# Performance work log

Hardware: AMD Instinct MI355X
Metric: run time of the kernel (lower is better)

## Reference

```python
import jax, jax.numpy as jnp
import numpy as np

N = 20000            # nodes
E = 320000           # edges (before self loops)
NUM_PLAYERS = 5000
FEAT = 64            # feature_dim
H = 128              # hidden_dim
OUT = 10             # out_features
NEG_SLOPE = 0.2


def _p(key, shape, fan_in):
    return jax.random.normal(key, shape, dtype=jnp.float32) / np.sqrt(fan_in)


def setup_inputs() -> dict:
    key = jax.random.key(0)
    ks = jax.random.split(key, 20)
    # x_player: col 0 = player id (stored as float), cols 1: = features
    ids = jax.random.randint(ks[0], (N, 1), 0, NUM_PLAYERS + 1).astype(jnp.float32)
    feats = jax.random.normal(ks[1], (N, FEAT), dtype=jnp.float32)
    x_player = jnp.concatenate([ids, feats], axis=1)
    edge_index = jax.random.randint(ks[2], (2, E), 0, N, dtype=jnp.int32)
    return {
        "x_player": x_player,
        "edge_index": edge_index,
        "emb": jax.random.normal(ks[3], (NUM_PLAYERS + 1, H), dtype=jnp.float32),
        "proj_W": _p(ks[4], (H + FEAT, H), H + FEAT),
        "proj_b": jnp.zeros((H,), jnp.float32),
        "W1l": _p(ks[5], (H, 4 * H), H),
        "W1r": _p(ks[6], (H, 4 * H), H),
        "att1": _p(ks[7], (4, H), H),
        "b1": jnp.zeros((4 * H,), jnp.float32),
        "W2l": _p(ks[8], (4 * H, H), 4 * H),
        "W2r": _p(ks[9], (4 * H, H), 4 * H),
        "att2": _p(ks[10], (1, H), H),
        "b2": jnp.zeros((H,), jnp.float32),
        "out_W": _p(ks[11], (H, OUT), H),
        "out_b": jnp.zeros((OUT,), jnp.float32),
    }


def gatv2(x, src, dst, Wl, Wr, att, bias, heads, ch, concat):
    # GATv2Conv (PyG defaults: share_weights=False, negative_slope=0.2,
    # add_self_loops handled by caller, dropout off at eval)
    xl = (x @ Wl).reshape(N, heads, ch)   # source transform (x_j)
    xr = (x @ Wr).reshape(N, heads, ch)   # target transform (x_i)
    h = xl[src] + xr[dst]                                      # [E,H,C]
    e = jnp.sum(jax.nn.leaky_relu(h, NEG_SLOPE) * att, -1)     # [E,H]
    # segment softmax over incoming edges of each dst node
    m = jax.ops.segment_max(e, dst, num_segments=N)            # [N,H]
    ex = jnp.exp(e - m[dst])
    s = jax.ops.segment_sum(ex, dst, num_segments=N)
    alpha = ex / (s[dst] + 1e-16)                              # [E,H]
    out = jax.ops.segment_sum(alpha[..., None] * xl[src], dst, num_segments=N)
    out = out.reshape(N, heads * ch) if concat else out.mean(axis=1)
    return out + bias


def reference(x_player, edge_index, emb, proj_W, proj_b,
              W1l, W1r, att1, b1, W2l, W2r, att2, b2, out_W, out_b):
    ids = x_player[:, 0].astype(jnp.int32)
    combined = jnp.concatenate([emb[ids], x_player[:, 1:]], axis=1)
    x = jax.nn.relu(combined @ proj_W + proj_b)                # [N,H]
    # add self loops (GATv2Conv default)
    loop = jnp.arange(N, dtype=edge_index.dtype)
    src = jnp.concatenate([edge_index[0], loop])
    dst = jnp.concatenate([edge_index[1], loop])
    x = jax.nn.relu(gatv2(x, src, dst, W1l, W1r, att1, b1, 4, H, True))
    x = gatv2(x, src, dst, W2l, W2r, att2, b2, 1, H, True)
    return x @ out_W + out_b                                   # [N,OUT]
```

## Files before the change

kernel.cpp:

```cpp
#include <hip/hip_runtime.h>
#include <math.h>

#define NNODES 20000
#define XP_COLS 65

typedef unsigned int uint32;
typedef __attribute__((ext_vector_type(8))) short short8;
typedef __attribute__((ext_vector_type(4))) float float4v;

__device__ __forceinline__ float bflo(uint32 u){ return __uint_as_float(u << 16); }
__device__ __forceinline__ float bfhi(uint32 u){ return __uint_as_float(u & 0xffff0000u); }
__device__ __forceinline__ unsigned short f2bf(float f){
  uint32 u = __float_as_uint(f);
  uint32 r = (u + 0x7fffu + ((u >> 16) & 1u)) >> 16;
  return (unsigned short)r;
}
__device__ __forceinline__ void unpack8(uint4 u, float* x){
  x[0]=bflo(u.x); x[1]=bfhi(u.x); x[2]=bflo(u.y); x[3]=bfhi(u.y);
  x[4]=bflo(u.z); x[5]=bfhi(u.z); x[6]=bflo(u.w); x[7]=bfhi(u.w);
}

__global__ void k_count(const int* __restrict__ dst, int E, int* __restrict__ deg){
  int e = blockIdx.x * 256 + threadIdx.x;
  if (e < E) atomicAdd(&deg[dst[e]], 1);
}

__global__ __launch_bounds__(256) void k_scan(const int* __restrict__ deg,
                                              int* __restrict__ off,
                                              int* __restrict__ cursor){
  const int CH = 80;
  int tid = threadIdx.x;
  int lane = tid & 63, w = tid >> 6;
  int beg = tid * CH;
  bool act = beg < NNODES;
  int sum = 0;
  if (act){
    const int4* p = (const int4*)(deg + beg);
    #pragma unroll
    for (int i = 0; i < 20; i++){
      int4 v = p[i];
      sum += v.x + v.y + v.z + v.w + 4;
    }
  }
  int inc = sum;
  #pragma unroll
  for (int d = 1; d < 64; d <<= 1){
    int t = __shfl_up(inc, d, 64);
    if (lane >= d) inc += t;
  }
  __shared__ int wtot[4];
  if (lane == 63) wtot[w] = inc;
  __syncthreads();
  int wbase = 0;
  for (int i = 0; i < w; i++) wbase += wtot[i];
  int run = wbase + inc - sum;
  if (act){
    const int4* p = (const int4*)(deg + beg);
    int4* po = (int4*)(off + beg);
    int4* pc = (int4*)(cursor + beg);
    #pragma unroll
    for (int i = 0; i < 20; i++){
      int4 v = p[i];
      int4 o;
      o.x = run; run += v.x + 1;
      o.y = run; run += v.y + 1;
      o.z = run; run += v.z + 1;
      o.w = run; run += v.w + 1;
      po[i] = o; pc[i] = o;
    }
  }
  if (tid == 249) off[NNODES] = run;
}

__global__ void k_fill(const int* __restrict__ src, const int* __restrict__ dst, int E,
                       int* __restrict__ cursor, int* __restrict__ csr){
  int t = blockIdx.x * 256 + threadIdx.x;
  if (t < NNODES){
    int p = atomicAdd(&cursor[t], 1);
    csr[p] = t;
  } else if (t < NNODES + E){
    int e = t - NNODES;
    int p = atomicAdd(&cursor[dst[e]], 1);
    csr[p] = src[e];
  }
}

__global__ void k_cvt(const float* __restrict__ W1l, const float* __restrict__ W1r,
                      const float* __restrict__ W2l, const float* __restrict__ W2r,
                      const float* __restrict__ projW,
                      unsigned short* __restrict__ T1l, unsigned short* __restrict__ T1r,
                      unsigned short* __restrict__ T2l, unsigned short* __restrict__ T2r,
                      unsigned short* __restrict__ Tp){
  int idx = blockIdx.x * 256 + threadIdx.x;
  if (idx < 65536){
    int o = idx;
    int n = o >> 7, k = o & 127;
    T1l[o] = f2bf(W1l[k * 512 + n]);
  } else if (idx < 131072){
    int o = idx - 65536;
    int n = o >> 7, k = o & 127;
    T1r[o] = f2bf(W1r[k * 512 + n]);
  } else if (idx < 196608){
    int o = idx - 131072;
    int n = o >> 9, k = o & 511;
    T2l[o] = f2bf(W2l[k * 128 + n]);
  } else if (idx < 262144){
    int o = idx - 196608;
    int n = o >> 9, k = o & 511;
    T2r[o] = f2bf(W2r[k * 128 + n]);
  } else if (idx < 286720){
    int o = idx - 262144;
    int n = o / 192, k = o - n * 192;
    Tp[o] = f2bf(projW[k * 128 + n]);
  }
}

__global__ __launch_bounds__(256) void k_proj_mfma(const float* __restrict__ xp,
                                                   const float* __restrict__ emb,
                                                   const unsigned short* __restrict__ Bt,
                                                   const float* __restrict__ bias,
                                                   unsigned short* __restrict__ Xb){
  __shared__ unsigned short As[64][40];
  __shared__ unsigned short Bs[128][40];
  __shared__ int ids[64];
  int tid = threadIdx.x;
  int bm = blockIdx.x * 64;
  int w = tid >> 6, lane = tid & 63;
  int wm = (w >> 1) * 32, wn = (w & 1) * 64;
  int quad = lane >> 4, l16 = lane & 15;
  if (tid < 64){
    int g = bm + tid;
    ids[tid] = (g < NNODES) ? (int)xp[(size_t)g * XP_COLS] : 0;
  }
  float4v acc[2][4];
  #pragma unroll
  for (int i = 0; i < 2; i++)
    #pragma unroll
    for (int j = 0; j < 4; j++) acc[i][j] = (float4v){0.f,0.f,0.f,0.f};
  int am = tid >> 2, ak = (tid & 3) * 8;
  int gm = bm + am;
  bool mv = gm < NNODES;
  int brow = tid >> 1, bk = (tid & 1) * 16;
  __syncthreads();

  for (int k0 = 0; k0 < 192; k0 += 32){
    float v[8];
    if (k0 < 128){
      const float* ep = emb + (size_t)ids[am] * 128 + k0 + ak;
      float4 e0 = *(const float4*)ep;
      float4 e1 = *(const float4*)(ep + 4);
      v[0]=e0.x; v[1]=e0.y; v[2]=e0.z; v[3]=e0.w;
      v[4]=e1.x; v[5]=e1.y; v[6]=e1.z; v[7]=e1.w;
    } else {
      const float* fp = xp + (size_t)gm * XP_COLS + 1 + (k0 - 128) + ak;
      #pragma unroll
      for (int i = 0; i < 8; i++) v[i] = mv ? fp[i] : 0.f;
    }
    ushort4 o0, o1;
    o0.x=f2bf(v[0]); o0.y=f2bf(v[1]); o0.z=f2bf(v[2]); o0.w=f2bf(v[3]);
    o1.x=f2bf(v[4]); o1.y=f2bf(v[5]); o1.z=f2bf(v[6]); o1.w=f2bf(v[7]);
    *(ushort4*)&As[am][ak]     = o0;
    *(ushort4*)&As[am][ak + 4] = o1;
    const unsigned short* bp = Bt + (size_t)brow * 192 + k0 + bk;
    *(uint4*)&Bs[brow][bk]     = *(const uint4*)bp;
    *(uint4*)&Bs[brow][bk + 8] = *(const uint4*)(bp + 8);
    __syncthreads();
    short8 af[2], bf[4];
    #pragma unroll
    for (int t = 0; t < 2; t++) af[t] = *(const short8*)&As[wm + t * 16 + l16][quad * 8];
    #pragma unroll
    for (int t = 0; t < 4; t++) bf[t] = *(const short8*)&Bs[wn + t * 16 + l16][quad * 8];
    #pragma unroll
    for (int tm = 0; tm < 2; tm++)
      #pragma unroll
      for (int tn = 0; tn < 4; tn++)
        acc[tm][tn] = __builtin_amdgcn_mfma_f32_16x16x32_bf16(af[tm], bf[tn], acc[tm][tn], 0, 0, 0);
    __syncthreads();
  }
  #pragma unroll
  for (int tm = 0; tm < 2; tm++){
    #pragma unroll
    for (int r = 0; r < 4; r++){
      int row = bm + wm + tm * 16 + quad * 4 + r;
      if (row >= NNODES) continue;
      #pragma unroll
      for (int tn = 0; tn < 4; tn++){
        int col = wn + tn * 16 + l16;
        float val = fmaxf(acc[tm][tn][r] + bias[col], 0.f);
        Xb[(size_t)row * 128 + col] = f2bf(val);
      }
    }
  }
}

template<int K, int N, int MODE, int NH>
__global__ __launch_bounds__(256) void k_mfma(const unsigned short* __restrict__ A,
                                              const unsigned short* __restrict__ B0t,
                                              const unsigned short* __restrict__ B1t,
                                              void* __restrict__ C0, void* __restrict__ C1,
                                              const float* __restrict__ att,
                                              float* __restrict__ dl, float* __restrict__ dr){
  const unsigned short* Bt = blockIdx.z ? B1t : B0t;
  __shared__ unsigned short As[64][40];
  __shared__ unsigned short Bs[128][40];
  __shared__ float red[4][32];
  int tid = threadIdx.x;
  int bm = blockIdx.y * 64;
  int bn = blockIdx.x * 128;
  int head = (NH == 1) ? 0 : blockIdx.x;
  int w = tid >> 6, lane = tid & 63;
  int wm = (w >> 1) * 32, wn = (w & 1) * 64;
  int quad = lane >> 4, l16 = lane & 15;
  float av[4];
  #pragma unroll
  for (int tn = 0; tn < 4; tn++) av[tn] = att[head * 128 + wn + tn * 16 + l16];
  float4v acc[2][4];
  #pragma unroll
  for (int i = 0; i < 2; i++)
    #pragma unroll
    for (int j = 0; j < 4; j++) acc[i][j] = (float4v){0.f,0.f,0.f,0.f};
  int am = tid >> 2, ak = (tid & 3) * 8;
  int gm = bm + am;
  bool mv = gm < NNODES;
  int brow = tid >> 1, bk = (tid & 1) * 16;

  for (int k0 = 0; k0 < K; k0 += 32){
    uint4 va = {0u,0u,0u,0u};
    if (mv) va = *(const uint4*)(A + (size_t)gm * K + k0 + ak);
    *(uint4*)&As[am][ak] = va;
    const unsigned short* bp = Bt + (size_t)(bn + brow) * K + k0 + bk;
    *(uint4*)&Bs[brow][bk]     = *(const uint4*)bp;
    *(uint4*)&Bs[brow][bk + 8] = *(const uint4*)(bp + 8);
    __syncthreads();
    short8 af[2], bf[4];
    #pragma unroll
    for (int t = 0; t < 2; t++) af[t] = *(const short8*)&As[wm + t * 16 + l16][quad * 8];
    #pragma unroll
    for (int t = 0; t < 4; t++) bf[t] = *(const short8*)&Bs[wn + t * 16 + l16][quad * 8];
    #pragma unroll
    for (int tm = 0; tm < 2; tm++)
      #pragma unroll
      for (int tn = 0; tn < 4; tn++)
        acc[tm][tn] = __builtin_amdgcn_mfma_f32_16x16x32_bf16(af[tm], bf[tn], acc[tm][tn], 0, 0, 0);
    __syncthreads();
  }
  #pragma unroll
  for (int tm = 0; tm < 2; tm++){
    #pragma unroll
    for (int r = 0; r < 4; r++){
      int row = bm + wm + tm * 16 + quad * 4 + r;
      if (row < NNODES){
        #pragma unroll
        for (int tn = 0; tn < 4; tn++){
          int col = bn + wn + tn * 16 + l16;
          float val = acc[tm][tn][r];
          if (MODE == 0 || blockIdx.z == 0){
            unsigned short* C = (unsigned short*)(blockIdx.z ? C1 : C0);
            C[(size_t)row * N + col] = f2bf(val);
          } else {
            ((float*)C1)[(size_t)row * N + col] = val;
          }
        }
      }
      float pd = acc[tm][0][r] * av[0];
      pd = fmaf(acc[tm][1][r], av[1], pd);
      pd = fmaf(acc[tm][2][r], av[2], pd);
      pd = fmaf(acc[tm][3][r], av[3], pd);
      pd += __shfl_xor(pd, 1);
      pd += __shfl_xor(pd, 2);
      pd += __shfl_xor(pd, 4);
      pd += __shfl_xor(pd, 8);
      if (l16 == 0) red[w][tm * 16 + quad * 4 + r] = pd;
    }
  }
  __syncthreads();
  if (tid < 64){
    float v = (tid < 32) ? red[0][tid] + red[1][tid] : red[2][tid & 31] + red[3][tid & 31];
    int row = bm + tid;
    if (row < NNODES){
      float* D = blockIdx.z ? dr : dl;
      D[row * NH + head] = v;
    }
  }
}

__global__ __launch_bounds__(256) void k_attn1(const unsigned short* __restrict__ xl,
                                               const unsigned short* __restrict__ xr,
                                               const float* __restrict__ dl, const float* __restrict__ dr,
                                               const float* __restrict__ att, const float* __restrict__ bias,
                                               const int* __restrict__ off, const int* __restrict__ csr,
                                               unsigned short* __restrict__ out){
  int lane = threadIdx.x & 63;
  int n = blockIdx.x * 4 + (threadIdx.x >> 6);
  int h = lane >> 4;
  uint4 ur = *(const uint4*)(xr + (size_t)n * 512 + lane * 8);
  float r[8]; unpack8(ur, r);
  const float* ap = att + lane * 8;
  float4 A0 = *(const float4*)ap, A1 = *(const float4*)(ap + 4);
  float a[8] = {A0.x,A0.y,A0.z,A0.w,A1.x,A1.y,A1.z,A1.w};
  float c0 = 0.6f * dr[n * 4 + h];
  int beg = off[n], end = off[n + 1];

  float m = -INFINITY, s = 0.f;
  float acc[8] = {0,0,0,0,0,0,0,0};
  int j = beg;
  for (; j + 3 < end; j += 4){
    int sn0 = csr[j], sn1 = csr[j + 1], sn2 = csr[j + 2], sn3 = csr[j + 3];
    uint4 u0 = *(const uint4*)(xl + (size_t)sn0 * 512 + lane * 8);
    uint4 u1 = *(const uint4*)(xl + (size_t)sn1 * 512 + lane * 8);
    uint4 u2 = *(const uint4*)(xl + (size_t)sn2 * 512 + lane * 8);
    uint4 u3 = *(const uint4*)(xl + (size_t)sn3 * 512 + lane * 8);
    float d0 = dl[sn0 * 4 + h], d1 = dl[sn1 * 4 + h];
    float d2 = dl[sn2 * 4 + h], d3 = dl[sn3 * 4 + h];
    float x0[8], x1[8], x2[8], x3[8];
    unpack8(u0, x0); unpack8(u1, x1); unpack8(u2, x2); unpack8(u3, x3);
    float p0 = 0.f, p1 = 0.f, p2 = 0.f, p3 = 0.f;
    #pragma unroll
    for (int i = 0; i < 8; i++){
      p0 = fmaf(a[i], fabsf(x0[i] + r[i]), p0);
      p1 = fmaf(a[i], fabsf(x1[i] + r[i]), p1);
      p2 = fmaf(a[i], fabsf(x2[i] + r[i]), p2);
      p3 = fmaf(a[i], fabsf(x3[i] + r[i]), p3);
    }
    p0 += __shfl_xor(p0, 1); p1 += __shfl_xor(p1, 1); p2 += __shfl_xor(p2, 1); p3 += __shfl_xor(p3, 1);
    p0 += __shfl_xor(p0, 2); p1 += __shfl_xor(p1, 2); p2 += __shfl_xor(p2, 2); p3 += __shfl_xor(p3, 2);
    p0 += __shfl_xor(p0, 4); p1 += __shfl_xor(p1, 4); p2 += __shfl_xor(p2, 4); p3 += __shfl_xor(p3, 4);
    p0 += __shfl_xor(p0, 8); p1 += __shfl_xor(p1, 8); p2 += __shfl_xor(p2, 8); p3 += __shfl_xor(p3, 8);
    float e0 = fmaf(0.6f, d0, fmaf(0.4f, p0, c0));
    float e1 = fmaf(0.6f, d1, fmaf(0.4f, p1, c0));
    float e2 = fmaf(0.6f, d2, fmaf(0.4f, p2, c0));
    float e3 = fmaf(0.6f, d3, fmaf(0.4f, p3, c0));
    float emax = fmaxf(fmaxf(e0, e1), fmaxf(e2, e3));
    if (__any(emax > m)){
      float nm = fmaxf(m, emax);
      float al  = __expf(m - nm);
      float ex0 = __expf(e0 - nm), ex1 = __expf(e1 - nm);
      float ex2 = __expf(e2 - nm), ex3 = __expf(e3 - nm);
      m = nm;
      s = fmaf(s, al, (ex0 + ex1) + (ex2 + ex3));
      #pragma unroll
      for (int i = 0; i < 8; i++){
        float t = fmaf(ex0, x0[i], ex1 * x1[i]);
        t = fmaf(ex2, x2[i], t);
        t = fmaf(ex3, x3[i], t);
        acc[i] = fmaf(acc[i], al, t);
      }
    } else {
      float ex0 = __expf(e0 - m), ex1 = __expf(e1 - m);
      float ex2 = __expf(e2 - m), ex3 = __expf(e3 - m);
      s += (ex0 + ex1) + (ex2 + ex3);
      #pragma unroll
      for (int i = 0; i < 8; i++){
        float t = fmaf(ex0, x0[i], ex1 * x1[i]);
        t = fmaf(ex2, x2[i], t);
        acc[i] = fmaf(ex3, x3[i], acc[i] + t);
      }
    }
  }
  for (; j < end; j++){
    int sn = csr[j];
    float dls = dl[sn * 4 + h];
    uint4 ux = *(const uint4*)(xl + (size_t)sn * 512 + lane * 8);
    float x[8]; unpack8(ux, x);
    float p = 0.f;
    #pragma unroll
    for (int i = 0; i < 8; i++) p = fmaf(a[i], fabsf(x[i] + r[i]), p);
    p += __shfl_xor(p, 1);
    p += __shfl_xor(p, 2);
    p += __shfl_xor(p, 4);
    p += __shfl_xor(p, 8);
    float e = fmaf(0.6f, dls, fmaf(0.4f, p, c0));
    if (__any(e > m)){
      float nm = fmaxf(m, e);
      float al = __expf(m - nm);
      float ex = __expf(e - nm);
      m = nm;
      s = fmaf(s, al, ex);
      #pragma unroll
      for (int i = 0; i < 8; i++) acc[i] = fmaf(acc[i], al, ex * x[i]);
    } else {
      float ex = __expf(e - m);
      s += ex;
      #pragma unroll
      for (int i = 0; i < 8; i++) acc[i] = fmaf(ex, x[i], acc[i]);
    }
  }
  float inv = 1.f / (s + 1e-16f);
  const float* bp = bias + lane * 8;
  float4 B0 = *(const float4*)bp, B1 = *(const float4*)(bp + 4);
  float bb[8] = {B0.x,B0.y,B0.z,B0.w,B1.x,B1.y,B1.z,B1.w};
  unsigned short o[8];
  #pragma unroll
  for (int i = 0; i < 8; i++)
    o[i] = f2bf(fmaxf(fmaf(acc[i], inv, bb[i]), 0.f));
  uint4 ov;
  ov.x = (uint32)o[0] | ((uint32)o[1] << 16);
  ov.y = (uint32)o[2] | ((uint32)o[3] << 16);
  ov.z = (uint32)o[4] | ((uint32)o[5] << 16);
  ov.w = (uint32)o[6] | ((uint32)o[7] << 16);
  *(uint4*)(out + (size_t)n * 512 + lane * 8) = ov;
}

__global__ __launch_bounds__(256) void k_attn2(const unsigned short* __restrict__ xl,
                                               const float* __restrict__ xr,
                                               const float* __restrict__ dl, const float* __restrict__ dr,
                                               const float* __restrict__ att, const float* __restrict__ bias,
                                               const float* __restrict__ outW, const float* __restrict__ outb,
                                               const int* __restrict__ off, const int* __restrict__ csr,
                                               float* __restrict__ out){
  __shared__ float Wsh[1280];
  int tid = threadIdx.x;
  for (int i = tid; i < 1280; i += 256) Wsh[i] = outW[i];
  __syncthreads();
  int lane = tid & 63;
  int n = blockIdx.x * 4 + (tid >> 6);
  float2 rv = *(const float2*)(xr + (size_t)n * 128 + lane * 2);
  float2 av = *(const float2*)(att + lane * 2);
  float c0 = 0.6f * dr[n];
  int beg = off[n], end = off[n + 1];
  float m = -INFINITY, s = 0.f;
  float a0 = 0.f, a1 = 0.f;
  int j = beg;
  for (; j + 3 < end; j += 4){
    int sn0 = csr[j], sn1 = csr[j + 1], sn2 = csr[j + 2], sn3 = csr[j + 3];
    uint32 u0 = *(const uint32*)(xl + (size_t)sn0 * 128 + lane * 2);
    uint32 u1 = *(const uint32*)(xl + (size_t)sn1 * 128 + lane * 2);
    uint32 u2 = *(const uint32*)(xl + (size_t)sn2 * 128 + lane * 2);
    uint32 u3 = *(const uint32*)(xl + (size_t)sn3 * 128 + lane * 2);
    float d0 = dl[sn0], d1 = dl[sn1], d2 = dl[sn2], d3 = dl[sn3];
    float x00 = bflo(u0), x01 = bfhi(u0);
    float x10 = bflo(u1), x11 = bfhi(u1);
    float x20 = bflo(u2), x21 = bfhi(u2);
    float x30 = bflo(u3), x31 = bfhi(u3);
    float p0 = fmaf(av.x, fabsf(x00 + rv.x), av.y * fabsf(x01 + rv.y));
    float p1 = fmaf(av.x, fabsf(x10 + rv.x), av.y * fabsf(x11 + rv.y));
    float p2 = fmaf(av.x, fabsf(x20 + rv.x), av.y * fabsf(x21 + rv.y));
    float p3 = fmaf(av.x, fabsf(x30 + rv.x), av.y * fabsf(x31 + rv.y));
    p0 += __shfl_xor(p0, 1);  p1 += __shfl_xor(p1, 1);  p2 += __shfl_xor(p2, 1);  p3 += __shfl_xor(p3, 1);
    p0 += __shfl_xor(p0, 2);  p1 += __shfl_xor(p1, 2);  p2 += __shfl_xor(p2, 2);  p3 += __shfl_xor(p3, 2);
    p0 += __shfl_xor(p0, 4);  p1 += __shfl_xor(p1, 4);  p2 += __shfl_xor(p2, 4);  p3 += __shfl_xor(p3, 4);
    p0 += __shfl_xor(p0, 8);  p1 += __shfl_xor(p1, 8);  p2 += __shfl_xor(p2, 8);  p3 += __shfl_xor(p3, 8);
    p0 += __shfl_xor(p0, 16); p1 += __shfl_xor(p1, 16); p2 += __shfl_xor(p2, 16); p3 += __shfl_xor(p3, 16);
    p0 += __shfl_xor(p0, 32); p1 += __shfl_xor(p1, 32); p2 += __shfl_xor(p2, 32); p3 += __shfl_xor(p3, 32);
    float e0 = fmaf(0.6f, d0, fmaf(0.4f, p0, c0));
    float e1 = fmaf(0.6f, d1, fmaf(0.4f, p1, c0));
    float e2 = fmaf(0.6f, d2, fmaf(0.4f, p2, c0));
    float e3 = fmaf(0.6f, d3, fmaf(0.4f, p3, c0));
    float emax = fmaxf(fmaxf(e0, e1), fmaxf(e2, e3));
    if (emax > m){
      float al  = __expf(m - emax);
      float ex0 = __expf(e0 - emax), ex1 = __expf(e1 - emax);
      float ex2 = __expf(e2 - emax), ex3 = __expf(e3 - emax);
      m = emax;
      s  = fmaf(s,  al, (ex0 + ex1) + (ex2 + ex3));
      float t0 = fmaf(ex0, x00, ex1 * x10); t0 = fmaf(ex2, x20, t0); t0 = fmaf(ex3, x30, t0);
      float t1 = fmaf(ex0, x01, ex1 * x11); t1 = fmaf(ex2, x21, t1); t1 = fmaf(ex3, x31, t1);
      a0 = fmaf(a0, al, t0);
      a1 = fmaf(a1, al, t1);
    } else {
      float ex0 = __expf(e0 - m), ex1 = __expf(e1 - m);
      float ex2 = __expf(e2 - m), ex3 = __expf(e3 - m);
      s += (ex0 + ex1) + (ex2 + ex3);
      float t0 = fmaf(ex0, x00, ex1 * x10); t0 = fmaf(ex2, x20, t0);
      float t1 = fmaf(ex0, x01, ex1 * x11); t1 = fmaf(ex2, x21, t1);
      a0 = fmaf(ex3, x30, a0 + t0);
      a1 = fmaf(ex3, x31, a1 + t1);
    }
  }
  for (; j < end; j++){
    int sn = csr[j];
    float dls = dl[sn];
    uint32 u = *(const uint32*)(xl + (size_t)sn * 128 + lane * 2);
    float x0 = bflo(u), x1 = bfhi(u);
    float p = fmaf(av.x, fabsf(x0 + rv.x), av.y * fabsf(x1 + rv.y));
    p += __shfl_xor(p, 1);
    p += __shfl_xor(p, 2);
    p += __shfl_xor(p, 4);
    p += __shfl_xor(p, 8);
    p += __shfl_xor(p, 16);
    p += __shfl_xor(p, 32);
    float e = fmaf(0.6f, dls, fmaf(0.4f, p, c0));
    if (e > m){
      float al = __expf(m - e);
      m = e;
      s  = fmaf(s,  al, 1.f);
      a0 = fmaf(a0, al, x0);
      a1 = fmaf(a1, al, x1);
    } else {
      float ex = __expf(e - m);
      s += ex;
      a0 = fmaf(ex, x0, a0);
      a1 = fmaf(ex, x1, a1);
    }
  }
  float inv = 1.f / (s + 1e-16f);
  int c = lane * 2;
  float x2_0 = fmaf(a0, inv, bias[c]);
  float x2_1 = fmaf(a1, inv, bias[c + 1]);
  #pragma unroll
  for (int o = 0; o < 10; o++){
    float p = fmaf(x2_0, Wsh[c * 10 + o], x2_1 * Wsh[(c + 1) * 10 + o]);
    p += __shfl_xor(p, 1);
    p += __shfl_xor(p, 2);
    p += __shfl_xor(p, 4);
    p += __shfl_xor(p, 8);
    p += __shfl_xor(p, 16);
    p += __shfl_xor(p, 32);
    if (lane == 0) out[(size_t)n * 10 + o] = p + outb[o];
  }
}

extern "C" void kernel_launch(void* const* d_in, const int* in_sizes, int n_in,
                              void* d_out, int out_size, void* d_ws, size_t ws_size,
                              hipStream_t stream){
  const float* xp    = (const float*)d_in[0];
  const int*   ei    = (const int*)  d_in[1];
  const float* emb   = (const float*)d_in[2];
  const float* projW = (const float*)d_in[3];
  const float* projb = (const float*)d_in[4];
  const float* W1l   = (const float*)d_in[5];
  const float* W1r   = (const float*)d_in[6];
  const float* att1  = (const float*)d_in[7];
  const float* b1    = (const float*)d_in[8];
  const float* W2l   = (const float*)d_in[9];
  const float* W2r   = (const float*)d_in[10];
  const float* att2  = (const float*)d_in[11];
  const float* b2    = (const float*)d_in[12];
  const float* outW  = (const float*)d_in[13];
  const float* outb  = (const float*)d_in[14];
  float* out = (float*)d_out;

  int E = in_sizes[1] / 2;
  const int* esrc = ei;
  const int* edst = ei + E;

  char* w = (char*)d_ws;
  int* deg  = (int*)w; w += (size_t)NNODES * 4;
  int* off  = (int*)w; w += (size_t)(NNODES + 4) * 4;
  int* cur  = (int*)w; w += (size_t)NNODES * 4;
  int* csr  = (int*)w; w += (size_t)(NNODES + E) * 4;
  unsigned short* Xb   = (unsigned short*)w; w += (size_t)NNODES * 128 * 2;
  unsigned short* Wt1l = (unsigned short*)w; w += (size_t)512 * 128 * 2;
  unsigned short* Wt1r = (unsigned short*)w; w += (size_t)512 * 128 * 2;
  unsigned short* Wt2l = (unsigned short*)w; w += (size_t)128 * 512 * 2;
  unsigned short* Wt2r = (unsigned short*)w; w += (size_t)128 * 512 * 2;
  unsigned short* Wtp  = (unsigned short*)w; w += (size_t)128 * 192 * 2;
  unsigned short* xl1b = (unsigned short*)w; w += (size_t)NNODES * 512 * 2;
  unsigned short* xr1b = (unsigned short*)w; w += (size_t)NNODES * 512 * 2;
  unsigned short* X1b  = (unsigned short*)w; w += (size_t)NNODES * 512 * 2;
  unsigned short* xl2b = (unsigned short*)w; w += (size_t)NNODES * 128 * 2;
  float* xr2 = (float*)w; w += (size_t)NNODES * 128 * 4;
  float* dl1 = (float*)w; w += (size_t)NNODES * 4 * 4;
  float* dr1 = (float*)w; w += (size_t)NNODES * 4 * 4;
  float* dl2 = (float*)w; w += (size_t)NNODES * 4;
  float* dr2 = (float*)w; w += (size_t)NNODES * 4;

  hipMemsetAsync(deg, 0, (size_t)NNODES * 4, stream);
  k_count<<<(E + 255) / 256, 256, 0, stream>>>(edst, E, deg);
  k_scan<<<1, 256, 0, stream>>>(deg, off, cur);
  k_fill<<<(NNODES + E + 255) / 256, 256, 0, stream>>>(esrc, edst, E, cur, csr);

  k_cvt<<<1120, 256, 0, stream>>>(W1l, W1r, W2l, W2r, projW, Wt1l, Wt1r, Wt2l, Wt2r, Wtp);
  k_proj_mfma<<<dim3((NNODES + 63) / 64), 256, 0, stream>>>(xp, emb, Wtp, projb, Xb);
  k_mfma<128, 512, 0, 4><<<dim3(4, (NNODES + 63) / 64, 2), 256, 0, stream>>>(
      Xb, Wt1l, Wt1r, xl1b, xr1b, att1, dl1, dr1);
  k_attn1<<<NNODES / 4, 256, 0, stream>>>(xl1b, xr1b, dl1, dr1, att1, b1, off, csr, X1b);
  k_mfma<512, 128, 1, 1><<<dim3(1, (NNODES + 63) / 64, 2), 256, 0, stream>>>(
      X1b, Wt2l, Wt2r, xl2b, xr2, att2, dl2, dr2);
  k_attn2<<<NNODES / 4, 256, 0, stream>>>(xl2b, xr2, dl2, dr2, att2, b2, outW, outb, off, csr, out);
}
```

Baseline: 300.1 us.

## Prefetch next neighbor batch in attention kernels and fuse weight convert with degree count

After: 298.0 us. About the same (-0.7%).

```diff
diff --git a/kernel.cpp b/kernel.cpp
--- a/kernel.cpp
+++ b/kernel.cpp
@@ -20,78 +20,19 @@
   x[4]=bflo(u.z); x[5]=bfhi(u.z); x[6]=bflo(u.w); x[7]=bfhi(u.w);
 }
 
-__global__ void k_count(const int* __restrict__ dst, int E, int* __restrict__ deg){
-  int e = blockIdx.x * 256 + threadIdx.x;
-  if (e < E) atomicAdd(&deg[dst[e]], 1);
-}
-
-__global__ __launch_bounds__(256) void k_scan(const int* __restrict__ deg,
-                                              int* __restrict__ off,
-                                              int* __restrict__ cursor){
-  const int CH = 80;
-  int tid = threadIdx.x;
-  int lane = tid & 63, w = tid >> 6;
-  int beg = tid * CH;
-  bool act = beg < NNODES;
-  int sum = 0;
-  if (act){
-    const int4* p = (const int4*)(deg + beg);
-    #pragma unroll
-    for (int i = 0; i < 20; i++){
-      int4 v = p[i];
-      sum += v.x + v.y + v.z + v.w + 4;
-    }
-  }
-  int inc = sum;
-  #pragma unroll
-  for (int d = 1; d < 64; d <<= 1){
-    int t = __shfl_up(inc, d, 64);
-    if (lane >= d) inc += t;
-  }
-  __shared__ int wtot[4];
-  if (lane == 63) wtot[w] = inc;
-  __syncthreads();
-  int wbase = 0;
-  for (int i = 0; i < w; i++) wbase += wtot[i];
-  int run = wbase + inc - sum;
-  if (act){
-    const int4* p = (const int4*)(deg + beg);
-    int4* po = (int4*)(off + beg);
-    int4* pc = (int4*)(cursor + beg);
-    #pragma unroll
-    for (int i = 0; i < 20; i++){
-      int4 v = p[i];
-      int4 o;
-      o.x = run; run += v.x + 1;
-      o.y = run; run += v.y + 1;
-      o.z = run; run += v.z + 1;
-      o.w = run; run += v.w + 1;
-      po[i] = o; pc[i] = o;
-    }
-  }
-  if (tid == 249) off[NNODES] = run;
-}
-
-__global__ void k_fill(const int* __restrict__ src, const int* __restrict__ dst, int E,
-                       int* __restrict__ cursor, int* __restrict__ csr){
-  int t = blockIdx.x * 256 + threadIdx.x;
-  if (t < NNODES){
-    int p = atomicAdd(&cursor[t], 1);
-    csr[p] = t;
-  } else if (t < NNODES + E){
-    int e = t - NNODES;
-    int p = atomicAdd(&cursor[dst[e]], 1);
-    csr[p] = src[e];
-  }
-}
-
-__global__ void k_cvt(const float* __restrict__ W1l, const float* __restrict__ W1r,
-                      const float* __restrict__ W2l, const float* __restrict__ W2r,
-                      const float* __restrict__ projW,
-                      unsigned short* __restrict__ T1l, unsigned short* __restrict__ T1r,
-                      unsigned short* __restrict__ T2l, unsigned short* __restrict__ T2r,
-                      unsigned short* __restrict__ Tp){
-  int idx = blockIdx.x * 256 + threadIdx.x;
+__global__ void k_cvt_count(const int* __restrict__ dst, int E, int* __restrict__ deg,
+                            const float* __restrict__ W1l, const float* __restrict__ W1r,
+                            const float* __restrict__ W2l, const float* __restrict__ W2r,
+                            const float* __restrict__ projW,
+                            unsigned short* __restrict__ T1l, unsigned short* __restrict__ T1r,
+                            unsigned short* __restrict__ T2l, unsigned short* __restrict__ T2r,
+                            unsigned short* __restrict__ Tp){
+  int gid = blockIdx.x * 256 + threadIdx.x;
+  if (gid < E){
+    atomicAdd(&deg[dst[gid]], 1);
+    return;
+  }
+  int idx = gid - E;
   if (idx < 65536){
     int o = idx;
     int n = o >> 7, k = o & 127;
@@ -112,6 +53,66 @@
     int o = idx - 262144;
     int n = o / 192, k = o - n * 192;
     Tp[o] = f2bf(projW[k * 128 + n]);
+  }
+}
+
+__global__ __launch_bounds__(256) void k_scan(const int* __restrict__ deg,
+                                              int* __restrict__ off,
+                                              int* __restrict__ cursor){
+  const int CH = 80;
+  int tid = threadIdx.x;
+  int lane = tid & 63, w = tid >> 6;
+  int beg = tid * CH;
+  bool act = beg < NNODES;
+  int sum = 0;
+  if (act){
+    const int4* p = (const int4*)(deg + beg);
+    #pragma unroll
+    for (int i = 0; i < 20; i++){
+      int4 v = p[i];
+      sum += v.x + v.y + v.z + v.w + 4;
+    }
+  }
+  int inc = sum;
+  #pragma unroll
+  for (int d = 1; d < 64; d <<= 1){
+    int t = __shfl_up(inc, d, 64);
+    if (lane >= d) inc += t;
+  }
+  __shared__ int wtot[4];
+  if (lane == 63) wtot[w] = inc;
+  __syncthreads();
+  int wbase = 0;
+  for (int i = 0; i < w; i++) wbase += wtot[i];
+  int run = wbase + inc - sum;
+  if (act){
+    const int4* p = (const int4*)(deg + beg);
+    int4* po = (int4*)(off + beg);
+    int4* pc = (int4*)(cursor + beg);
+    #pragma unroll
+    for (int i = 0; i < 20; i++){
+      int4 v = p[i];
+      int4 o;
+      o.x = run; run += v.x + 1;
+      o.y = run; run += v.y + 1;
+      o.z = run; run += v.z + 1;
+      o.w = run; run += v.w + 1;
+      po[i] = o; pc[i] = o;
+    }
+  }
+  if (tid == 249) off[NNODES] = run;
+}
+
+__global__ void k_fill(const int* __restrict__ src, const int* __restrict__ dst, int E,
+                       int* __restrict__ cursor, int* __restrict__ csr){
+  int t = blockIdx.x * 256 + threadIdx.x;
+  if (t < NNODES){
+    int p = atomicAdd(&cursor[t], 1);
+    csr[p] = t;
+  } else if (t < NNODES + E){
+    int e = t - NNODES;
+    int p = atomicAdd(&cursor[dst[e]], 1);
+    csr[p] = src[e];
   }
 }
 
@@ -284,6 +285,55 @@
   }
 }
 
+__device__ __forceinline__ void attn1_batch(const uint4* u, const float* d,
+                                            const float* r, const float* a, float c0,
+                                            float& m, float& s, float* acc){
+  float x0[8], x1[8], x2[8], x3[8];
+  unpack8(u[0], x0); unpack8(u[1], x1); unpack8(u[2], x2); unpack8(u[3], x3);
+  float p0 = 0.f, p1 = 0.f, p2 = 0.f, p3 = 0.f;
+  #pragma unroll
+  for (int i = 0; i < 8; i++){
+    p0 = fmaf(a[i], fabsf(x0[i] + r[i]), p0);
+    p1 = fmaf(a[i], fabsf(x1[i] + r[i]), p1);
+    p2 = fmaf(a[i], fabsf(x2[i] + r[i]), p2);
+    p3 = fmaf(a[i], fabsf(x3[i] + r[i]), p3);
+  }
+  p0 += __shfl_xor(p0, 1); p1 += __shfl_xor(p1, 1); p2 += __shfl_xor(p2, 1); p3 += __shfl_xor(p3, 1);
+  p0 += __shfl_xor(p0, 2); p1 += __shfl_xor(p1, 2); p2 += __shfl_xor(p2, 2); p3 += __shfl_xor(p3, 2);
+  p0 += __shfl_xor(p0, 4); p1 += __shfl_xor(p1, 4); p2 += __shfl_xor(p2, 4); p3 += __shfl_xor(p3, 4);
+  p0 += __shfl_xor(p0, 8); p1 += __shfl_xor(p1, 8); p2 += __shfl_xor(p2, 8); p3 += __shfl_xor(p3, 8);
+  float e0 = fmaf(0.6f, d[0], fmaf(0.4f, p0, c0));
+  float e1 = fmaf(0.6f, d[1], fmaf(0.4f, p1, c0));
+  float e2 = fmaf(0.6f, d[2], fmaf(0.4f, p2, c0));
+  float e3 = fmaf(0.6f, d[3], fmaf(0.4f, p3, c0));
+  float emax = fmaxf(fmaxf(e0, e1), fmaxf(e2, e3));
+  if (__any(emax > m)){
+    float nm = fmaxf(m, emax);
+    float al  = __expf(m - nm);
+    float ex0 = __expf(e0 - nm), ex1 = __expf(e1 - nm);
+    float ex2 = __expf(e2 - nm), ex3 = __expf(e3 - nm);
+    m = nm;
+    s = fmaf(s, al, (ex0 + ex1) + (ex2 + ex3));
+    #pragma unroll
+    for (int i = 0; i < 8; i++){
+      float t = fmaf(ex0, x0[i], ex1 * x1[i]);
+      t = fmaf(ex2, x2[i], t);
+      t = fmaf(ex3, x3[i], t);
+      acc[i] = fmaf(acc[i], al, t);
+    }
+  } else {
+    float ex0 = __expf(e0 - m), ex1 = __expf(e1 - m);
+    float ex2 = __expf(e2 - m), ex3 = __expf(e3 - m);
+    s += (ex0 + ex1) + (ex2 + ex3);
+    #pragma unroll
+    for (int i = 0; i < 8; i++){
+      float t = fmaf(ex0, x0[i], ex1 * x1[i]);
+      t = fmaf(ex2, x2[i], t);
+      acc[i] = fmaf(ex3, x3[i], acc[i] + t);
+    }
+  }
+}
+
 __global__ __launch_bounds__(256) void k_attn1(const unsigned short* __restrict__ xl,
                                                const unsigned short* __restrict__ xr,
                                                const float* __restrict__ dl, const float* __restrict__ dr,
@@ -300,62 +350,36 @@
   float a[8] = {A0.x,A0.y,A0.z,A0.w,A1.x,A1.y,A1.z,A1.w};
   float c0 = 0.6f * dr[n * 4 + h];
   int beg = off[n], end = off[n + 1];
+  int cnt = end - beg;
+  int nfull = cnt >> 2;
 
   float m = -INFINITY, s = 0.f;
   float acc[8] = {0,0,0,0,0,0,0,0};
+  uint4 uA[4], uB[4];
+  float dA[4], dB[4];
   int j = beg;
-  for (; j + 3 < end; j += 4){
-    int sn0 = csr[j], sn1 = csr[j + 1], sn2 = csr[j + 2], sn3 = csr[j + 3];
-    uint4 u0 = *(const uint4*)(xl + (size_t)sn0 * 512 + lane * 8);
-    uint4 u1 = *(const uint4*)(xl + (size_t)sn1 * 512 + lane * 8);
-    uint4 u2 = *(const uint4*)(xl + (size_t)sn2 * 512 + lane * 8);
-    uint4 u3 = *(const uint4*)(xl + (size_t)sn3 * 512 + lane * 8);
-    float d0 = dl[sn0 * 4 + h], d1 = dl[sn1 * 4 + h];
-    float d2 = dl[sn2 * 4 + h], d3 = dl[sn3 * 4 + h];
-    float x0[8], x1[8], x2[8], x3[8];
-    unpack8(u0, x0); unpack8(u1, x1); unpack8(u2, x2); unpack8(u3, x3);
-    float p0 = 0.f, p1 = 0.f, p2 = 0.f, p3 = 0.f;
-    #pragma unroll
-    for (int i = 0; i < 8; i++){
-      p0 = fmaf(a[i], fabsf(x0[i] + r[i]), p0);
-      p1 = fmaf(a[i], fabsf(x1[i] + r[i]), p1);
-      p2 = fmaf(a[i], fabsf(x2[i] + r[i]), p2);
-      p3 = fmaf(a[i], fabsf(x3[i] + r[i]), p3);
-    }
-    p0 += __shfl_xor(p0, 1); p1 += __shfl_xor(p1, 1); p2 += __shfl_xor(p2, 1); p3 += __shfl_xor(p3, 1);
-    p0 += __shfl_xor(p0, 2); p1 += __shfl_xor(p1, 2); p2 += __shfl_xor(p2, 2); p3 += __shfl_xor(p3, 2);
-    p0 += __shfl_xor(p0, 4); p1 += __shfl_xor(p1, 4); p2 += __shfl_xor(p2, 4); p3 += __shfl_xor(p3, 4);
-    p0 += __shfl_xor(p0, 8); p1 += __shfl_xor(p1, 8); p2 += __shfl_xor(p2, 8); p3 += __shfl_xor(p3, 8);
-    float e0 = fmaf(0.6f, d0, fmaf(0.4f, p0, c0));
-    float e1 = fmaf(0.6f, d1, fmaf(0.4f, p1, c0));
-    float e2 = fmaf(0.6f, d2, fmaf(0.4f, p2, c0));
-    float e3 = fmaf(0.6f, d3, fmaf(0.4f, p3, c0));
-    float emax = fmaxf(fmaxf(e0, e1), fmaxf(e2, e3));
-    if (__any(emax > m)){
-      float nm = fmaxf(m, emax);
-      float al  = __expf(m - nm);
-      float ex0 = __expf(e0 - nm), ex1 = __expf(e1 - nm);
-      float ex2 = __expf(e2 - nm), ex3 = __expf(e3 - nm);
-      m = nm;
-      s = fmaf(s, al, (ex0 + ex1) + (ex2 + ex3));
-      #pragma unroll
-      for (int i = 0; i < 8; i++){
-        float t = fmaf(ex0, x0[i], ex1 * x1[i]);
-        t = fmaf(ex2, x2[i], t);
-        t = fmaf(ex3, x3[i], t);
-        acc[i] = fmaf(acc[i], al, t);
-      }
-    } else {
-      float ex0 = __expf(e0 - m), ex1 = __expf(e1 - m);
-      float ex2 = __expf(e2 - m), ex3 = __expf(e3 - m);
-      s += (ex0 + ex1) + (ex2 + ex3);
-      #pragma unroll
-      for (int i = 0; i < 8; i++){
-        float t = fmaf(ex0, x0[i], ex1 * x1[i]);
-        t = fmaf(ex2, x2[i], t);
-        acc[i] = fmaf(ex3, x3[i], acc[i] + t);
-      }
-    }
+  if (nfull > 0){
+    int s0 = csr[j], s1 = csr[j+1], s2 = csr[j+2], s3 = csr[j+3];
+    uA[0] = *(const uint4*)(xl + (size_t)s0 * 512 + lane * 8);
+    uA[1] = *(const uint4*)(xl + (size_t)s1 * 512 + lane * 8);
+    uA[2] = *(const uint4*)(xl + (size_t)s2 * 512 + lane * 8);
+    uA[3] = *(const uint4*)(xl + (size_t)s3 * 512 + lane * 8);
+    dA[0] = dl[s0*4+h]; dA[1] = dl[s1*4+h]; dA[2] = dl[s2*4+h]; dA[3] = dl[s3*4+h];
+  }
+  for (int b = 0; b < nfull; b++){
+    int jn = j + 4;
+    if (b + 1 < nfull){
+      int s0 = csr[jn], s1 = csr[jn+1], s2 = csr[jn+2], s3 = csr[jn+3];
+      uB[0] = *(const uint4*)(xl + (size_t)s0 * 512 + lane * 8);
+      uB[1] = *(const uint4*)(xl + (size_t)s1 * 512 + lane * 8);
+      uB[2] = *(const uint4*)(xl + (size_t)s2 * 512 + lane * 8);
+      uB[3] = *(const uint4*)(xl + (size_t)s3 * 512 + lane * 8);
+      dB[0] = dl[s0*4+h]; dB[1] = dl[s1*4+h]; dB[2] = dl[s2*4+h]; dB[3] = dl[s3*4+h];
+    }
+    attn1_batch(uA, dA, r, a, c0, m, s, acc);
+    j = jn;
+    #pragma unroll
+    for (int i = 0; i < 4; i++){ uA[i] = uB[i]; dA[i] = dB[i]; }
   }
   for (; j < end; j++){
     int sn = csr[j];
@@ -401,6 +425,49 @@
   *(uint4*)(out + (size_t)n * 512 + lane * 8) = ov;
 }
 
+__device__ __forceinline__ void attn2_batch(const uint32* u, const float* d,
+                                            float2 rv, float2 av, float c0,
+                                            float& m, float& s, float& a0, float& a1){
+  float x00 = bflo(u[0]), x01 = bfhi(u[0]);
+  float x10 = bflo(u[1]), x11 = bfhi(u[1]);
+  float x20 = bflo(u[2]), x21 = bfhi(u[2]);
+  float x30 = bflo(u[3]), x31 = bfhi(u[3]);
+  float p0 = fmaf(av.x, fabsf(x00 + rv.x), av.y * fabsf(x01 + rv.y));
+  float p1 = fmaf(av.x, fabsf(x10 + rv.x), av.y * fabsf(x11 + rv.y));
+  float p2 = fmaf(av.x, fabsf(x20 + rv.x), av.y * fabsf(x21 + rv.y));
+  float p3 = fmaf(av.x, fabsf(x30 + rv.x), av.y * fabsf(x31 + rv.y));
+  p0 += __shfl_xor(p0, 1);  p1 += __shfl_xor(p1, 1);  p2 += __shfl_xor(p2, 1);  p3 += __shfl_xor(p3, 1);
+  p0 += __shfl_xor(p0, 2);  p1 += __shfl_xor(p1, 2);  p2 += __shfl_xor(p2, 2);  p3 += __shfl_xor(p3, 2);
+  p0 += __shfl_xor(p0, 4);  p1 += __shfl_xor(p1, 4);  p2 += __shfl_xor(p2, 4);  p3 += __shfl_xor(p3, 4);
+  p0 += __shfl_xor(p0, 8);  p1 += __shfl_xor(p1, 8);  p2 += __shfl_xor(p2, 8);  p3 += __shfl_xor(p3, 8);
+  p0 += __shfl_xor(p0, 16); p1 += __shfl_xor(p1, 16); p2 += __shfl_xor(p2, 16); p3 += __shfl_xor(p3, 16);
+  p0 += __shfl_xor(p0, 32); p1 += __shfl_xor(p1, 32); p2 += __shfl_xor(p2, 32); p3 += __shfl_xor(p3, 32);
+  float e0 = fmaf(0.6f, d[0], fmaf(0.4f, p0, c0));
+  float e1 = fmaf(0.6f, d[1], fmaf(0.4f, p1, c0));
+  float e2 = fmaf(0.6f, d[2], fmaf(0.4f, p2, c0));
+  float e3 = fmaf(0.6f, d[3], fmaf(0.4f, p3, c0));
+  float emax = fmaxf(fmaxf(e0, e1), fmaxf(e2, e3));
+  if (emax > m){
+    float al  = __expf(m - emax);
+    float ex0 = __expf(e0 - emax), ex1 = __expf(e1 - emax);
+    float ex2 = __expf(e2 - emax), ex3 = __expf(e3 - emax);
+    m = emax;
+    s  = fmaf(s,  al, (ex0 + ex1) + (ex2 + ex3));
+    float t0 = fmaf(ex0, x00, ex1 * x10); t0 = fmaf(ex2, x20, t0); t0 = fmaf(ex3, x30, t0);
+    float t1 = fmaf(ex0, x01, ex1 * x11); t1 = fmaf(ex2, x21, t1); t1 = fmaf(ex3, x31, t1);
+    a0 = fmaf(a0, al, t0);
+    a1 = fmaf(a1, al, t1);
+  } else {
+    float ex0 = __expf(e0 - m), ex1 = __expf(e1 - m);
+    float ex2 = __expf(e2 - m), ex3 = __expf(e3 - m);
+    s += (ex0 + ex1) + (ex2 + ex3);
+    float t0 = fmaf(ex0, x00, ex1 * x10); t0 = fmaf(ex2, x20, t0);
+    float t1 = fmaf(ex0, x01, ex1 * x11); t1 = fmaf(ex2, x21, t1);
+    a0 = fmaf(ex3, x30, a0 + t0);
+    a1 = fmaf(ex3, x31, a1 + t1);
+  }
+}
+
 __global__ __launch_bounds__(256) void k_attn2(const unsigned short* __restrict__ xl,
                                                const float* __restrict__ xr,
                                                const float* __restrict__ dl, const float* __restrict__ dr,
@@ -418,54 +485,35 @@
   float2 av = *(const float2*)(att + lane * 2);
   float c0 = 0.6f * dr[n];
   int beg = off[n], end = off[n + 1];
+  int cnt = end - beg;
+  int nfull = cnt >> 2;
   float m = -INFINITY, s = 0.f;
   float a0 = 0.f, a1 = 0.f;
+  uint32 uA[4], uB[4];
+  float dA[4], dB[4];
   int j = beg;
-  for (; j + 3 < end; j += 4){
-    int sn0 = csr[j], sn1 = csr[j + 1], sn2 = csr[j + 2], sn3 = csr[j + 3];
-    uint32 u0 = *(const uint32*)(xl + (size_t)sn0 * 128 + lane * 2);
-    uint32 u1 = *(const uint32*)(xl + (size_t)sn1 * 128 + lane * 2);
-    uint32 u2 = *(const uint32*)(xl + (size_t)sn2 * 128 + lane * 2);
-    uint32 u3 = *(const uint32*)(xl + (size_t)sn3 * 128 + lane * 2);
-    float d0 = dl[sn0], d1 = dl[sn1], d2 = dl[sn2], d3 = dl[sn3];
-    float x00 = bflo(u0), x01 = bfhi(u0);
-    float x10 = bflo(u1), x11 = bfhi(u1);
-    float x20 = bflo(u2), x21 = bfhi(u2);
-    float x30 = bflo(u3), x31 = bfhi(u3);
-    float p0 = fmaf(av.x, fabsf(x00 + rv.x), av.y * fabsf(x01 + rv.y));
-    float p1 = fmaf(av.x, fabsf(x10 + rv.x), av.y * fabsf(x11 + rv.y));
-    float p2 = fmaf(av.x, fabsf(x20 + rv.x), av.y * fabsf(x21 + rv.y));
-    float p3 = fmaf(av.x, fabsf(x30 + rv.x), av.y * fabsf(x31 + rv.y));
-    p0 += __shfl_xor(p0, 1);  p1 += __shfl_xor(p1, 1);  p2 += __shfl_xor(p2, 1);  p3 += __shfl_xor(p3, 1);
-    p0 += __shfl_xor(p0, 2);  p1 += __shfl_xor(p1, 2);  p2 += __shfl_xor(p2, 2);  p3 += __shfl_xor(p3, 2);
-    p0 += __shfl_xor(p0, 4);  p1 += __shfl_xor(p1, 4);  p2 += __shfl_xor(p2, 4);  p3 += __shfl_xor(p3, 4);
-    p0 += __shfl_xor(p0, 8);  p1 += __shfl_xor(p1, 8);  p2 += __shfl_xor(p2, 8);  p3 += __shfl_xor(p3, 8);
-    p0 += __shfl_xor(p0, 16); p1 += __shfl_xor(p1, 16); p2 += __shfl_xor(p2, 16); p3 += __shfl_xor(p3, 16);
-    p0 += __shfl_xor(p0, 32); p1 += __shfl_xor(p1, 32); p2 += __shfl_xor(p2, 32); p3 += __shfl_xor(p3, 32);
-    float e0 = fmaf(0.6f, d0, fmaf(0.4f, p0, c0));
-    float e1 = fmaf(0.6f, d1, fmaf(0.4f, p1, c0));
-    float e2 = fmaf(0.6f, d2, fmaf(0.4f, p2, c0));
-    float e3 = fmaf(0.6f, d3, fmaf(0.4f, p3, c0));
-    float emax = fmaxf(fmaxf(e0, e1), fmaxf(e2, e3));
-    if (emax > m){
-      float al  = __expf(m - emax);
-      float ex0 = __expf(e0 - emax), ex1 = __expf(e1 - emax);
-      float ex2 = __expf(e2 - emax), ex3 = __expf(e3 - emax);
-      m = emax;
-      s  = fmaf(s,  al, (ex0 + ex1) + (ex2 + ex3));
-      float t0 = fmaf(ex0, x00, ex1 * x10); t0 = fmaf(ex2, x20, t0); t0 = fmaf(ex3, x30, t0);
-      float t1 = fmaf(ex0, x01, ex1 * x11); t1 = fmaf(ex2, x21, t1); t1 = fmaf(ex3, x31, t1);
-      a0 = fmaf(a0, al, t0);
-      a1 = fmaf(a1, al, t1);
-    } else {
-      float ex0 = __expf(e0 - m), ex1 = __expf(e1 - m);
-      float ex2 = __expf(e2 - m), ex3 = __expf(e3 - m);
-      s += (ex0 + ex1) + (ex2 + ex3);
-      float t0 = fmaf(ex0, x00, ex1 * x10); t0 = fmaf(ex2, x20, t0);
-      float t1 = fmaf(ex0, x01, ex1 * x11); t1 = fmaf(ex2, x21, t1);
-      a0 = fmaf(ex3, x30, a0 + t0);
-      a1 = fmaf(ex3, x31, a1 + t1);
-    }
+  if (nfull > 0){
+    int s0 = csr[j], s1 = csr[j+1], s2 = csr[j+2], s3 = csr[j+3];
+    uA[0] = *(const uint32*)(xl + (size_t)s0 * 128 + lane * 2);
+    uA[1] = *(const uint32*)(xl + (size_t)s1 * 128 + lane * 2);
+    uA[2] = *(const uint32*)(xl + (size_t)s2 * 128 + lane * 2);
+    uA[3] = *(const uint32*)(xl + (size_t)s3 * 128 + lane * 2);
+    dA[0] = dl[s0]; dA[1] = dl[s1]; dA[2] = dl[s2]; dA[3] = dl[s3];
+  }
+  for (int b = 0; b < nfull; b++){
+    int jn = j + 4;
+    if (b + 1 < nfull){
+      int s0 = csr[jn], s1 = csr[jn+1], s2 = csr[jn+2], s3 = csr[jn+3];
+      uB[0] = *(const uint32*)(xl + (size_t)s0 * 128 + lane * 2);
+      uB[1] = *(const uint32*)(xl + (size_t)s1 * 128 + lane * 2);
+      uB[2] = *(const uint32*)(xl + (size_t)s2 * 128 + lane * 2);
+      uB[3] = *(const uint32*)(xl + (size_t)s3 * 128 + lane * 2);
+      dB[0] = dl[s0]; dB[1] = dl[s1]; dB[2] = dl[s2]; dB[3] = dl[s3];
+    }
+    attn2_batch(uA, dA, rv, av, c0, m, s, a0, a1);
+    j = jn;
+    #pragma unroll
+    for (int i = 0; i < 4; i++){ uA[i] = uB[i]; dA[i] = dB[i]; }
   }
   for (; j < end; j++){
     int sn = csr[j];
@@ -556,11 +604,12 @@
   float* dr2 = (float*)w; w += (size_t)NNODES * 4;
 
   hipMemsetAsync(deg, 0, (size_t)NNODES * 4, stream);
-  k_count<<<(E + 255) / 256, 256, 0, stream>>>(edst, E, deg);
+  int cvt_total = E + 286720;
+  k_cvt_count<<<(cvt_total + 255) / 256, 256, 0, stream>>>(
+      edst, E, deg, W1l, W1r, W2l, W2r, projW, Wt1l, Wt1r, Wt2l, Wt2r, Wtp);
   k_scan<<<1, 256, 0, stream>>>(deg, off, cur);
   k_fill<<<(NNODES + E + 255) / 256, 256, 0, stream>>>(esrc, edst, E, cur, csr);
 
-  k_cvt<<<1120, 256, 0, stream>>>(W1l, W1r, W2l, W2r, projW, Wt1l, Wt1r, Wt2l, Wt2r, Wtp);
   k_proj_mfma<<<dim3((NNODES + 63) / 64), 256, 0, stream>>>(xp, emb, Wtp, projb, Xb);
   k_mfma<128, 512, 0, 4><<<dim3(4, (NNODES + 63) / 64, 2), 256, 0, stream>>>(
       Xb, Wt1l, Wt1r, xl1b, xr1b, att1, dl1, dr1);
```
